# Kernel tuning notes

Measured on AMD Instinct MI355X. Metric: run time of the kernel, lower is better.

## Reference

```python
import jax, jax.numpy as jnp
import numpy as np

B, N, C, H, W = 2, 512, 32, 200, 200
THRESH = 0.05
# BEVCamera: x_range=y_range=(-1,1) -> FoV=2 meters; sh = H/FoVy = 100, sw = W/FoVx = 100
SH = H / 2.0
SW = W / 2.0
LOWPASS = 0.3        # 3DGS low-pass filter added to 2D cov diagonal
ALPHA_MIN = 1.0 / 255.0
ALPHA_MAX = 0.99


def setup_inputs() -> dict:
    key = jax.random.key(0)
    k1, k2, k3, k4 = jax.random.split(key, 4)
    features = jax.random.normal(k1, (B, N, C), dtype=jnp.float32)
    means3D = jax.random.uniform(k2, (B, N, 3), dtype=jnp.float32, minval=-1.0, maxval=1.0)
    # build PSD 3D covariances: Sigma = A A^T + eps*I, store 6 upper-tri entries
    A = 0.05 * jax.random.normal(k3, (B, N, 3, 3), dtype=jnp.float32)
    S = jnp.einsum('bnij,bnkj->bnik', A, A) + 1e-4 * jnp.eye(3, dtype=jnp.float32)
    cov3D = jnp.stack([S[..., 0, 0], S[..., 0, 1], S[..., 0, 2],
                       S[..., 1, 1], S[..., 1, 2], S[..., 2, 2]], axis=-1)
    opacities = jax.random.uniform(k4, (B, N, 1), dtype=jnp.float32)
    return {"features": features, "means3D": means3D, "cov3D": cov3D, "opacities": opacities}


def _render_one(features, means3D, cov3D, op):
    # features [N,C], means3D [N,3], cov3D [N,6] (xx,xy,xz,yy,yz,zz), op [N,1]
    dtype = features.dtype
    opac = op[:, 0]
    opac = jnp.where(opac > THRESH, opac, 0.0)  # masked-out gaussians contribute nothing
    # projmatrix: u = H/2 - sh*y (height), v = W/2 - sw*x (width)
    mu_u = H / 2.0 - SH * means3D[:, 1]
    mu_v = W / 2.0 - SW * means3D[:, 0]
    # 2D covariance from orthographic BEV projection J = [[0,-sh,0],[-sw,0,0]]
    Cuu = SH * SH * cov3D[:, 3] + LOWPASS
    Cvv = SW * SW * cov3D[:, 0] + LOWPASS
    Cuv = SH * SW * cov3D[:, 1]
    det = Cuu * Cvv - Cuv * Cuv
    valid = det > 0.0
    inv_det = jnp.where(valid, 1.0 / jnp.where(valid, det, 1.0), 0.0)
    Iuu = Cvv * inv_det
    Ivv = Cuu * inv_det
    Iuv = -Cuv * inv_det
    opac = jnp.where(valid, opac, 0.0)
    uu = jnp.arange(H, dtype=dtype)
    vv = jnp.arange(W, dtype=dtype)
    du = uu[None, :, None] - mu_u[:, None, None]   # [N,H,1]
    dv = vv[None, None, :] - mu_v[:, None, None]   # [N,1,W]
    power = (-0.5 * (Iuu[:, None, None] * du * du + Ivv[:, None, None] * dv * dv)
             - Iuv[:, None, None] * du * dv)       # [N,H,W]
    alpha = jnp.minimum(ALPHA_MAX, opac[:, None, None] * jnp.exp(jnp.minimum(power, 0.0)))
    alpha = jnp.where((power > 0.0) | (alpha < ALPHA_MIN), 0.0, alpha)
    # front-to-back alpha compositing in gaussian index order (all depths are 0 -> stable sort)
    logt = jnp.log1p(-alpha)                       # [N,H,W]
    T = jnp.exp(jnp.cumsum(logt, axis=0) - logt)   # exclusive transmittance
    w = T * alpha                                  # [N,H,W]
    return jnp.einsum('nhw,nc->chw', w, features)  # bg color is zeros


def reference(features, means3D, cov3D, opacities):
    bev = jax.vmap(_render_one)(features, means3D, cov3D, opacities)  # [B,C,H,W]
    num_gaussians = (opacities[..., 0] > THRESH).astype(jnp.float32).sum(axis=-1).mean()
    return bev, num_gaussians
```

## Files before the change

### kernel.cpp

```cpp
#include <hip/hip_runtime.h>
#include <math.h>

#define B_ 2
#define N_ 512
#define C_ 32
#define H_ 200
#define W_ 200
#define HW_ (H_*W_)
#define THRESH_ 0.05f
#define OUT_BEV (B_*C_*H_*W_)
#define NSEG 4
#define TILES_PER_B 625
#define LOG2E 1.4426950408889634f
#define LN2   0.6931471805599453f

typedef float v2f __attribute__((ext_vector_type(2)));

__device__ __forceinline__ float rlane(float x, int l) {
    return __int_as_float(__builtin_amdgcn_readlane(__float_as_int(x), l));
}

__device__ __forceinline__ bool pcompute(
    const float* __restrict__ m3, const float* __restrict__ cv,
    const float* __restrict__ opc, int i,
    float tu0, float tu1, float tv0, float tv1,
    float& mu_u, float& mu_v, float& a2, float& b2, float& c2,
    float& opo, float& thr2)
{
    float x  = m3[i*3 + 0];
    float y  = m3[i*3 + 1];
    float c0 = cv[i*6 + 0];
    float c1 = cv[i*6 + 1];
    float c3 = cv[i*6 + 3];
    float op = opc[i];
    mu_u = 100.0f - 100.0f * y;
    mu_v = 100.0f - 100.0f * x;
    float Cuu = 10000.0f * c3 + 0.3f;
    float Cvv = 10000.0f * c0 + 0.3f;
    float Cuv = 10000.0f * c1;
    float det = Cuu * Cvv - Cuv * Cuv;
    bool valid = det > 0.0f;
    float opac = (op > THRESH_) ? op : 0.0f;
    if (!valid) opac = 0.0f;
    float inv_det = valid ? (1.0f / det) : 0.0f;
    a2 = -0.5f * LOG2E * (Cvv * inv_det);
    b2 = -0.5f * LOG2E * (Cuu * inv_det);
    c2 =  LOG2E * (Cuv * inv_det);
    opo = opac;
    if (opac > 0.0f) {
        float r2 = log2f(255.0f * opac);
        thr2 = -r2;
        float rn = LN2 * r2;
        float du_max = sqrtf(fmaxf(2.0f * rn * Cuu, 0.0f)) + 1.0e-3f;
        float dv_max = sqrtf(fmaxf(2.0f * rn * Cvv, 0.0f)) + 1.0e-3f;
        return (mu_u - du_max <= tu1) & (mu_u + du_max >= tu0) &
               (mu_v - dv_max <= tv1) & (mu_v + dv_max >= tv0);
    }
    thr2 = 3.0e38f;
    return false;
}

#define WALK(mask, P, base_n)                                                \
    while (mask) {                                                           \
        int j0 = __builtin_ctzll(mask); mask &= mask - 1;                    \
        bool two = (mask != 0ull);                                           \
        int j1 = two ? __builtin_ctzll(mask) : j0;                           \
        if (two) mask &= mask - 1;                                           \
        float mu_u0 = rlane(P##_mu_u, j0), mu_v0 = rlane(P##_mu_v, j0);      \
        float a0 = rlane(P##_a, j0), b0 = rlane(P##_b, j0);                  \
        float c0 = rlane(P##_c, j0), op0 = rlane(P##_op, j0);                \
        float th0 = rlane(P##_th, j0);                                       \
        float mu_u1 = rlane(P##_mu_u, j1), mu_v1 = rlane(P##_mu_v, j1);      \
        float a1 = rlane(P##_a, j1), b1 = rlane(P##_b, j1);                  \
        float c1 = rlane(P##_c, j1), op1 = rlane(P##_op, j1);                \
        float th1 = rlane(P##_th, j1);                                       \
        const v2f* f0 = (const v2f*)(featB + (size_t)((base_n) + j0) * C_);  \
        const v2f* f1 = (const v2f*)(featB + (size_t)((base_n) + j1) * C_);  \
        float du0 = u - mu_u0, dv0 = v - mu_v0;                              \
        float pw0 = fmaf(a0 * du0, du0, fmaf(b0 * dv0, dv0, c0 * (du0 * dv0))); \
        bool hit0 = (pw0 <= 0.0f) && (pw0 >= th0);                           \
        float al0 = hit0 ? fminf(0.99f, op0 * exp2f(pw0)) : 0.0f;            \
        float du1 = u - mu_u1, dv1 = v - mu_v1;                              \
        float pw1 = fmaf(a1 * du1, du1, fmaf(b1 * dv1, dv1, c1 * (du1 * dv1))); \
        bool hit1 = two && (pw1 <= 0.0f) && (pw1 >= th1);                    \
        float al1 = hit1 ? fminf(0.99f, op1 * exp2f(pw1)) : 0.0f;            \
        if (__any(hit0 | hit1)) {                                            \
            float w0 = T * al0;                                              \
            float Tm = T * (1.0f - al0);                                     \
            float w1 = Tm * al1;                                             \
            T = Tm * (1.0f - al1);                                           \
            v2f w0v = {w0, w0}, w1v = {w1, w1};                              \
            _Pragma("unroll")                                                \
            for (int i = 0; i < 16; ++i)                                     \
                acc2[i] = __builtin_elementwise_fma(w1v, f1[i],              \
                          __builtin_elementwise_fma(w0v, f0[i], acc2[i]));   \
        }                                                                    \
    }

__global__ __launch_bounds__(256, 5) void render_kernel(
    const float* __restrict__ features,
    const float* __restrict__ means3D,
    const float* __restrict__ cov3D,
    const float* __restrict__ opacities,
    float* __restrict__ out)
{
    __shared__ float s_T[NSEG][64];
    __shared__ unsigned int s_pk[NSEG * 16 * 64];

    int blk = blockIdx.x;
    int tid = threadIdx.x;

    if (blk == B_ * TILES_PER_B) {
        int cnt = ((opacities[tid]       > THRESH_) ? 1 : 0)
                + ((opacities[tid + 256] > THRESH_) ? 1 : 0)
                + ((opacities[tid + 512] > THRESH_) ? 1 : 0)
                + ((opacities[tid + 768] > THRESH_) ? 1 : 0);
        for (int off = 32; off > 0; off >>= 1) cnt += __shfl_down(cnt, off);
        int* s_red = (int*)s_T;
        if ((tid & 63) == 0) s_red[tid >> 6] = cnt;
        __syncthreads();
        if (tid == 0)
            out[OUT_BEV] = (float)(s_red[0] + s_red[1] + s_red[2] + s_red[3]) * 0.5f;
        return;
    }

    int b  = blk / TILES_PER_B;
    int t  = blk - b * TILES_PER_B;
    int tu = t / 25;
    int tv = t - tu * 25;
    int wave = __builtin_amdgcn_readfirstlane(tid >> 6);
    int lane = tid & 63;

    float tu0 = (float)(tu * 8), tu1 = tu0 + 7.0f;
    float tv0 = (float)(tv * 8), tv1 = tv0 + 7.0f;

    float A_mu_u, A_mu_v, A_a, A_b, A_c, A_op, A_th;
    float B_mu_u, B_mu_v, B_a, B_b, B_c, B_op, B_th;
    int i0 = b * N_ + wave * 128 + lane;
    bool ovA = pcompute(means3D, cov3D, opacities, i0,      tu0, tu1, tv0, tv1,
                        A_mu_u, A_mu_v, A_a, A_b, A_c, A_op, A_th);
    bool ovB = pcompute(means3D, cov3D, opacities, i0 + 64, tu0, tu1, tv0, tv1,
                        B_mu_u, B_mu_v, B_a, B_b, B_c, B_op, B_th);
    unsigned long long m0 = __ballot(ovA);
    unsigned long long m1 = __ballot(ovB);

    int uu = tu * 8 + (lane >> 3);
    int vv = tv * 8 + (lane & 7);
    float u = (float)uu, v = (float)vv;

    float T = 1.0f;
    v2f acc2[16];
#pragma unroll
    for (int i = 0; i < 16; ++i) acc2[i] = (v2f){0.0f, 0.0f};
    const float* featB = features + (size_t)b * (N_ * C_);

    WALK(m0, A, wave * 128)
    WALK(m1, B, wave * 128 + 64)

    s_T[wave][lane] = T;
#pragma unroll
    for (int i = 0; i < 16; ++i) {
        unsigned int r;
        asm("v_cvt_pk_bf16_f32 %0, %1, %2"
            : "=v"(r) : "v"(acc2[i].x), "v"(acc2[i].y));
        s_pk[(wave * 16 + i) * 64 + lane] = r;
    }
    __syncthreads();

    float t0g = s_T[0][lane], t1g = s_T[1][lane], t2g = s_T[2][lane];
    float Wg[NSEG];
    Wg[0] = 1.0f;
    Wg[1] = t0g;
    Wg[2] = t0g * t1g;
    Wg[3] = Wg[2] * t2g;

    size_t obase = (size_t)b * C_ * HW_ + (size_t)(tu * 8) * W_ + (size_t)(tv * 8);
    size_t opix  = (size_t)(lane >> 3) * W_ + (lane & 7);
#pragma unroll
    for (int q = 0; q < 4; ++q) {
        int pr = wave * 4 + q;
        float vlo = 0.0f, vhi = 0.0f;
#pragma unroll
        for (int g = 0; g < NSEG; ++g) {
            unsigned int r = s_pk[(g * 16 + pr) * 64 + lane];
            float flo = __uint_as_float(r << 16);
            float fhi = __uint_as_float(r & 0xffff0000u);
            vlo = fmaf(Wg[g], flo, vlo);
            vhi = fmaf(Wg[g], fhi, vhi);
        }
        out[obase + (size_t)(2 * pr)     * HW_ + opix] = vlo;
        out[obase + (size_t)(2 * pr + 1) * HW_ + opix] = vhi;
    }
}

extern "C" void kernel_launch(void* const* d_in, const int* in_sizes, int n_in,
                              void* d_out, int out_size, void* d_ws, size_t ws_size,
                              hipStream_t stream) {
    const float* features  = (const float*)d_in[0];
    const float* means3D   = (const float*)d_in[1];
    const float* cov3D     = (const float*)d_in[2];
    const float* opacities = (const float*)d_in[3];
    float* out = (float*)d_out;
    render_kernel<<<B_ * TILES_PER_B + 1, 256, 0, stream>>>(
        features, means3D, cov3D, opacities, out);
}
```

Baseline: 16.84 us.

## Use exact ellipse-vs-tile overlap test and spiral tile order from center

Result: faster. 16.50 us, median of 2 (-2.0%).

```diff
diff --git a/kernel.cpp b/kernel.cpp
--- a/kernel.cpp
+++ b/kernel.cpp
@@ -20,12 +20,11 @@
     return __int_as_float(__builtin_amdgcn_readlane(__float_as_int(x), l));
 }
 
-__device__ __forceinline__ bool pcompute(
+__device__ __forceinline__ void pcompute(
     const float* __restrict__ m3, const float* __restrict__ cv,
     const float* __restrict__ opc, int i,
-    float tu0, float tu1, float tv0, float tv1,
     float& mu_u, float& mu_v, float& a2, float& b2, float& c2,
-    float& opo, float& thr2)
+    float& opo, float& thr2, float& inv2a, float& inv2b)
 {
     float x  = m3[i*3 + 0];
     float y  = m3[i*3 + 1];
@@ -48,17 +47,43 @@
     c2 =  LOG2E * (Cuv * inv_det);
     opo = opac;
     if (opac > 0.0f) {
-        float r2 = log2f(255.0f * opac);
-        thr2 = -r2;
-        float rn = LN2 * r2;
-        float du_max = sqrtf(fmaxf(2.0f * rn * Cuu, 0.0f)) + 1.0e-3f;
-        float dv_max = sqrtf(fmaxf(2.0f * rn * Cvv, 0.0f)) + 1.0e-3f;
-        return (mu_u - du_max <= tu1) & (mu_u + du_max >= tu0) &
-               (mu_v - dv_max <= tv1) & (mu_v + dv_max >= tv0);
-    }
-    thr2 = 3.0e38f;
-    return false;
-}
+        thr2 = -log2f(255.0f * opac);
+        inv2a = 1.0f / (2.0f * a2);
+        inv2b = 1.0f / (2.0f * b2);
+    } else {
+        thr2 = 3.0e38f;
+        inv2a = 0.0f;
+        inv2b = 0.0f;
+    }
+}
+
+__device__ __forceinline__ float edge_max_u(float a2, float b2, float c2,
+                                            float due, float dvlo, float dvhi,
+                                            float inv2b) {
+    float dvs = fminf(fmaxf(-c2 * due * inv2b, dvlo), dvhi);
+    return fmaf(a2 * due, due, fmaf(b2 * dvs, dvs, c2 * (due * dvs)));
+}
+__device__ __forceinline__ float edge_max_v(float a2, float b2, float c2,
+                                            float dve, float dulo, float duhi,
+                                            float inv2a) {
+    float dus = fminf(fmaxf(-c2 * dve * inv2a, dulo), duhi);
+    return fmaf(a2 * dus, dus, fmaf(b2 * dve, dve, c2 * (dus * dve)));
+}
+
+#define OVTEST(P, ovname)                                                     \
+    bool ovname;                                                              \
+    {                                                                         \
+        float dulo = tu0 - P##_mu_u, duhi = tu1 - P##_mu_u;                   \
+        float dvlo = tv0 - P##_mu_v, dvhi = tv1 - P##_mu_v;                   \
+        bool inside = (dulo <= 0.0f) & (duhi >= 0.0f) &                       \
+                      (dvlo <= 0.0f) & (dvhi >= 0.0f);                        \
+        float e0 = edge_max_u(P##_a, P##_b, P##_c, dulo, dvlo, dvhi, P##_i2b);\
+        float e1 = edge_max_u(P##_a, P##_b, P##_c, duhi, dvlo, dvhi, P##_i2b);\
+        float e2 = edge_max_v(P##_a, P##_b, P##_c, dvlo, dulo, duhi, P##_i2a);\
+        float e3 = edge_max_v(P##_a, P##_b, P##_c, dvhi, dulo, duhi, P##_i2a);\
+        float mx = fmaxf(fmaxf(e0, e1), fmaxf(e2, e3));                       \
+        ovname = (P##_op > 0.0f) && (inside || (mx >= P##_th));               \
+    }
 
 #define WALK(mask, P, base_n)                                                \
     while (mask) {                                                           \
@@ -124,23 +149,41 @@
         return;
     }
 
-    int b  = blk / TILES_PER_B;
-    int t  = blk - b * TILES_PER_B;
-    int tu = t / 25;
-    int tv = t - tu * 25;
+    int b = blk & 1;
+    int i = blk >> 1;
+    int s = (int)sqrtf((float)i);
+    int r = (s + 1) >> 1;
+    int tu, tv;
+    if (r == 0) {
+        tu = 12; tv = 12;
+    } else {
+        int base = (2 * r - 1) * (2 * r - 1);
+        int p  = i - base;
+        int tr = 2 * r;
+        int side = p / tr;
+        int off  = p - side * tr;
+        if      (side == 0) { tu = 12 - r + off; tv = 12 - r; }
+        else if (side == 1) { tu = 12 + r;       tv = 12 - r + off; }
+        else if (side == 2) { tu = 12 + r - off; tv = 12 + r; }
+        else                { tu = 12 - r;       tv = 12 + r - off; }
+    }
+
     int wave = __builtin_amdgcn_readfirstlane(tid >> 6);
     int lane = tid & 63;
 
     float tu0 = (float)(tu * 8), tu1 = tu0 + 7.0f;
     float tv0 = (float)(tv * 8), tv1 = tv0 + 7.0f;
 
-    float A_mu_u, A_mu_v, A_a, A_b, A_c, A_op, A_th;
-    float B_mu_u, B_mu_v, B_a, B_b, B_c, B_op, B_th;
+    float A_mu_u, A_mu_v, A_a, A_b, A_c, A_op, A_th, A_i2a, A_i2b;
+    float B_mu_u, B_mu_v, B_a, B_b, B_c, B_op, B_th, B_i2a, B_i2b;
     int i0 = b * N_ + wave * 128 + lane;
-    bool ovA = pcompute(means3D, cov3D, opacities, i0,      tu0, tu1, tv0, tv1,
-                        A_mu_u, A_mu_v, A_a, A_b, A_c, A_op, A_th);
-    bool ovB = pcompute(means3D, cov3D, opacities, i0 + 64, tu0, tu1, tv0, tv1,
-                        B_mu_u, B_mu_v, B_a, B_b, B_c, B_op, B_th);
+    pcompute(means3D, cov3D, opacities, i0,
+             A_mu_u, A_mu_v, A_a, A_b, A_c, A_op, A_th, A_i2a, A_i2b);
+    pcompute(means3D, cov3D, opacities, i0 + 64,
+             B_mu_u, B_mu_v, B_a, B_b, B_c, B_op, B_th, B_i2a, B_i2b);
+
+    OVTEST(A, ovA)
+    OVTEST(B, ovB)
     unsigned long long m0 = __ballot(ovA);
     unsigned long long m1 = __ballot(ovB);
 
@@ -151,7 +194,7 @@
     float T = 1.0f;
     v2f acc2[16];
 #pragma unroll
-    for (int i = 0; i < 16; ++i) acc2[i] = (v2f){0.0f, 0.0f};
+    for (int i2 = 0; i2 < 16; ++i2) acc2[i2] = (v2f){0.0f, 0.0f};
     const float* featB = features + (size_t)b * (N_ * C_);
 
     WALK(m0, A, wave * 128)
@@ -159,11 +202,11 @@
 
     s_T[wave][lane] = T;
 #pragma unroll
-    for (int i = 0; i < 16; ++i) {
-        unsigned int r;
+    for (int i2 = 0; i2 < 16; ++i2) {
+        unsigned int rr;
         asm("v_cvt_pk_bf16_f32 %0, %1, %2"
-            : "=v"(r) : "v"(acc2[i].x), "v"(acc2[i].y));
-        s_pk[(wave * 16 + i) * 64 + lane] = r;
+            : "=v"(rr) : "v"(acc2[i2].x), "v"(acc2[i2].y));
+        s_pk[(wave * 16 + i2) * 64 + lane] = rr;
     }
     __syncthreads();
 
@@ -182,9 +225,9 @@
         float vlo = 0.0f, vhi = 0.0f;
 #pragma unroll
         for (int g = 0; g < NSEG; ++g) {
-            unsigned int r = s_pk[(g * 16 + pr) * 64 + lane];
-            float flo = __uint_as_float(r << 16);
-            float fhi = __uint_as_float(r & 0xffff0000u);
+            unsigned int rr = s_pk[(g * 16 + pr) * 64 + lane];
+            float flo = __uint_as_float(rr << 16);
+            float fhi = __uint_as_float(rr & 0xffff0000u);
             vlo = fmaf(Wg[g], flo, vlo);
             vhi = fmaf(Wg[g], fhi, vhi);
         }
```
